# Performance work log

Hardware: AMD Instinct MI355X
Metric: run time of the kernel (lower is better)

## Reference

```python
import jax, jax.numpy as jnp
import numpy as np
import math

IN_CH = 256
RED_CH = 32  # max(256//8, 32)

def setup_inputs() -> dict:
    key = jax.random.key(0)
    k1, k2, k3, k4, k5 = jax.random.split(key, 5)
    x = jax.random.normal(k1, (2, IN_CH, 8, 28, 28), dtype=jnp.float32)
    # 1x1x1 Conv3d weights, kaiming-normal style scale (fan_out)
    def kaiming(k, shape):
        fan_out = shape[0]
        std = math.sqrt(2.0 / fan_out)
        return jax.random.normal(k, shape, dtype=jnp.float32) * std
    q_w = kaiming(k2, (RED_CH, IN_CH))
    k_w = kaiming(k3, (RED_CH, IN_CH))
    v_w = kaiming(k4, (RED_CH, IN_CH))
    out_w = kaiming(k5, (IN_CH, RED_CH))
    return {"x": x, "q_w": q_w, "k_w": k_w, "v_w": v_w, "out_w": out_w}

def reference(x, q_w, k_w, v_w, out_w):
    b, c, t, h, w = x.shape
    n = t * h * w
    xf = x.reshape(b, c, n)  # [B, C, N] (1x1x1 conv == channel matmul)
    q = jnp.einsum('rc,bcn->brn', q_w, xf)  # [B, Cr, N]
    k = jnp.einsum('rc,bcn->brn', k_w, xf)
    v = jnp.einsum('rc,bcn->brn', v_w, xf)
    scale = 1.0 / math.sqrt(RED_CH)
    attn = jnp.einsum('bri,brj->bij', q, k) * scale  # [B, N, N]
    attn = jax.nn.softmax(attn, axis=2)
    out = jnp.einsum('brj,bij->bri', v, attn)  # [B, Cr, N]
    out = jnp.einsum('cr,brn->bcn', out_w, out).reshape(b, c, t, h, w)
    return x + out
```

## Files before the change

kernel.cpp:

```cpp
#include <hip/hip_runtime.h>
#include <hip/hip_bf16.h>

#define NPOS 6272
#define NT   98
#define CIN  256
#define CR   32
#define BATCH 2
#define QS2  0.25503371989518595f
#define PPITCH 72

typedef short bf16x8s __attribute__((ext_vector_type(8)));
typedef short short4v __attribute__((ext_vector_type(4)));
typedef float f32x4   __attribute__((ext_vector_type(4)));
typedef unsigned short ushort_t;

__device__ __forceinline__ ushort_t f2bf(float f) {
    unsigned u = __builtin_bit_cast(unsigned, f);
    u += 0x7fff + ((u >> 16) & 1);
    return (ushort_t)(u >> 16);
}
__device__ __forceinline__ float bf2f(ushort_t h) {
    return __builtin_bit_cast(float, (unsigned)h << 16);
}
__device__ __forceinline__ ushort_t f2bf_hw(float f) {
    __bf16 b = (__bf16)f;
    return __builtin_bit_cast(ushort_t, b);
}

__global__ __launch_bounds__(256) void qkv_kernel(
    const float* __restrict__ x, const float* __restrict__ qw,
    const float* __restrict__ kw, const float* __restrict__ vw,
    ushort_t* __restrict__ Qh, ushort_t* __restrict__ Ql,
    ushort_t* __restrict__ Kh, ushort_t* __restrict__ Kl,
    ushort_t* __restrict__ Vt)
{
    const int b   = blockIdx.y;
    const int z   = blockIdx.z;
    const int nl  = threadIdx.x & 63;
    const int n   = blockIdx.x * 64 + nl;
    const int g   = __builtin_amdgcn_readfirstlane(threadIdx.x >> 6);
    const float* w  = (z == 0) ? qw : (z == 1) ? kw : vw;
    const float* xb = x + (size_t)b * CIN * NPOS + n;

    float acc[8];
#pragma unroll
    for (int i = 0; i < 8; ++i) acc[i] = 0.f;
#pragma unroll 8
    for (int c = 0; c < CIN; ++c) {
        float xv = xb[(size_t)c * NPOS];
#pragma unroll
        for (int i = 0; i < 8; ++i)
            acc[i] += w[(g * 8 + i) * CIN + c] * xv;
    }
    if (z == 2) {
#pragma unroll
        for (int i = 0; i < 8; ++i)
            Vt[((size_t)b * CR + g * 8 + i) * NPOS + n] = f2bf(acc[i]);
    } else {
        ushort_t* dh = (z == 0) ? Qh : Kh;
        ushort_t* dl = (z == 0) ? Ql : Kl;
        float s = (z == 0) ? QS2 : 1.0f;
        bf16x8s fh, fl;
#pragma unroll
        for (int i = 0; i < 8; ++i) {
            float v = acc[i] * s;
            ushort_t h = f2bf(v);
            fh[i] = (short)h;
            fl[i] = (short)f2bf(v - bf2f(h));
        }
        size_t off = ((size_t)b * NPOS + n) * CR + g * 8;
        *(bf16x8s*)(dh + off) = fh;
        *(bf16x8s*)(dl + off) = fl;
    }
}

__device__ __forceinline__ void load_tile(
    const ushort_t* __restrict__ Khb, const ushort_t* __restrict__ Klb,
    const ushort_t* __restrict__ Vtb, int j0, int col, int quad,
    bf16x8s* kh, bf16x8s* kl, bf16x8s* vb)
{
#pragma unroll
    for (int f = 0; f < 4; ++f) {
        kh[f] = *(const bf16x8s*)(Khb + (size_t)(j0 + f * 16 + col) * CR + quad * 8);
        kl[f] = *(const bf16x8s*)(Klb + (size_t)(j0 + f * 16 + col) * CR + quad * 8);
    }
#pragma unroll
    for (int k2 = 0; k2 < 2; ++k2)
#pragma unroll
        for (int c = 0; c < 2; ++c)
            vb[k2 * 2 + c] = *(const bf16x8s*)(
                Vtb + (size_t)(c * 16 + col) * NPOS + j0 + k2 * 32 + quad * 8);
}

__device__ __forceinline__ void compute_tile(
    const bf16x8s* kh, const bf16x8s* kl, const bf16x8s* vb,
    const bf16x8s* qbh, const bf16x8s* qbl,
    f32x4 (&oc)[2][2], float (&m_)[2], float (&l_)[2],
    ushort_t* pb, int col, int quad)
{
    f32x4 z4 = {0.f, 0.f, 0.f, 0.f};
#pragma unroll
    for (int h = 0; h < 2; ++h) {
        f32x4 sc[4];
#pragma unroll
        for (int f = 0; f < 4; ++f) {
            sc[f] = __builtin_amdgcn_mfma_f32_16x16x32_bf16(kl[f], qbh[h], z4, 0, 0, 0);
            sc[f] = __builtin_amdgcn_mfma_f32_16x16x32_bf16(kh[f], qbl[h], sc[f], 0, 0, 0);
            sc[f] = __builtin_amdgcn_mfma_f32_16x16x32_bf16(kh[f], qbh[h], sc[f], 0, 0, 0);
        }
        float a0 = fmaxf(fmaxf(sc[0][0], sc[0][1]), sc[0][2]);
        float a1 = fmaxf(fmaxf(sc[0][3], sc[1][0]), sc[1][1]);
        float a2 = fmaxf(fmaxf(sc[1][2], sc[1][3]), sc[2][0]);
        float a3 = fmaxf(fmaxf(sc[2][1], sc[2][2]), sc[2][3]);
        float a4 = fmaxf(fmaxf(sc[3][0], sc[3][1]), sc[3][2]);
        float b0 = fmaxf(fmaxf(a0, a1), a2);
        float b1 = fmaxf(fmaxf(a3, a4), sc[3][3]);
        float v  = fmaxf(b0, b1);
        v = fmaxf(v, __shfl_xor(v, 16));
        v = fmaxf(v, __shfl_xor(v, 32));
        float mo = m_[h];
        float mn = mo;
        if (!__all(v <= mo)) {
            mn = fmaxf(mo, v);
            float al = __builtin_amdgcn_exp2f(mo - mn);
            m_[h] = mn;
            l_[h] *= al;
#pragma unroll
            for (int r = 0; r < 4; ++r) { oc[h][0][r] *= al; oc[h][1][r] *= al; }
        }
        float lsum = 0.f;
#pragma unroll
        for (int f = 0; f < 4; ++f) {
            float p0 = __builtin_amdgcn_exp2f(sc[f][0] - mn);
            float p1 = __builtin_amdgcn_exp2f(sc[f][1] - mn);
            float p2 = __builtin_amdgcn_exp2f(sc[f][2] - mn);
            float p3 = __builtin_amdgcn_exp2f(sc[f][3] - mn);
            lsum += (p0 + p1) + (p2 + p3);
            short4v pk;
            pk[0] = (short)f2bf_hw(p0);
            pk[1] = (short)f2bf_hw(p1);
            pk[2] = (short)f2bf_hw(p2);
            pk[3] = (short)f2bf_hw(p3);
            *(short4v*)(&pb[h * 16 * PPITCH + col * PPITCH + f * 16 + quad * 4]) = pk;
        }
        l_[h] += lsum;
    }
#pragma unroll
    for (int h = 0; h < 2; ++h) {
#pragma unroll
        for (int k2 = 0; k2 < 2; ++k2) {
            bf16x8s pbo = *(const bf16x8s*)(
                &pb[h * 16 * PPITCH + col * PPITCH + k2 * 32 + quad * 8]);
            oc[h][0] = __builtin_amdgcn_mfma_f32_16x16x32_bf16(vb[k2 * 2 + 0], pbo, oc[h][0], 0, 0, 0);
            oc[h][1] = __builtin_amdgcn_mfma_f32_16x16x32_bf16(vb[k2 * 2 + 1], pbo, oc[h][1], 0, 0, 0);
        }
    }
}

template <int ITERS>
__global__ __launch_bounds__(128, 2) void attn_kernel(
    const ushort_t* __restrict__ Qh, const ushort_t* __restrict__ Ql,
    const ushort_t* __restrict__ Kh, const ushort_t* __restrict__ Kl,
    const ushort_t* __restrict__ Vt, ushort_t* __restrict__ Opart,
    float* __restrict__ Mp, float* __restrict__ Lp)
{
    __shared__ __align__(16) ushort_t pbuf[2 * 2 * 16 * PPITCH];

    const int lane = threadIdx.x & 63;
    const int wv   = threadIdx.x >> 6;
    const int col  = lane & 15;
    const int quad = lane >> 4;
    const int b    = blockIdx.z;
    const int s    = blockIdx.y;
    const int qw0  = blockIdx.x * 64 + wv * 32;
    ushort_t* pb   = &pbuf[wv * 2 * 16 * PPITCH];

    const ushort_t* Qhb = Qh + (size_t)b * NPOS * CR;
    const ushort_t* Qlb = Ql + (size_t)b * NPOS * CR;
    const ushort_t* Khb = Kh + (size_t)b * NPOS * CR;
    const ushort_t* Klb = Kl + (size_t)b * NPOS * CR;
    const ushort_t* Vtb = Vt + (size_t)b * CR * NPOS;

    bf16x8s qbh[2], qbl[2];
    qbh[0] = *(const bf16x8s*)(Qhb + (size_t)(qw0 + col) * CR + quad * 8);
    qbh[1] = *(const bf16x8s*)(Qhb + (size_t)(qw0 + 16 + col) * CR + quad * 8);
    qbl[0] = *(const bf16x8s*)(Qlb + (size_t)(qw0 + col) * CR + quad * 8);
    qbl[1] = *(const bf16x8s*)(Qlb + (size_t)(qw0 + 16 + col) * CR + quad * 8);

    f32x4 oc[2][2];
#pragma unroll
    for (int h = 0; h < 2; ++h)
#pragma unroll
        for (int c = 0; c < 2; ++c)
#pragma unroll
            for (int r = 0; r < 4; ++r) oc[h][c][r] = 0.f;
    float m_[2] = { -1e30f, -1e30f };
    float l_[2] = { 0.f, 0.f };

    if constexpr (ITERS <= 14) {
        bf16x8s kh2[2][4], kl2[2][4], vb2[2][4];
        load_tile(Khb, Klb, Vtb, s * ITERS * 64, col, quad,
                  kh2[0], kl2[0], vb2[0]);
#pragma unroll
        for (int it = 0; it < ITERS; ++it) {
            const int cur = it & 1;
            if (it + 1 < ITERS)
                load_tile(Khb, Klb, Vtb, (s * ITERS + it + 1) * 64, col, quad,
                          kh2[cur ^ 1], kl2[cur ^ 1], vb2[cur ^ 1]);
            compute_tile(kh2[cur], kl2[cur], vb2[cur], qbh, qbl, oc, m_, l_,
                         pb, col, quad);
        }
    } else {
        for (int it = 0; it < ITERS; ++it) {
            bf16x8s kh[4], kl[4], vb[4];
            load_tile(Khb, Klb, Vtb, (s * ITERS + it) * 64, col, quad, kh, kl, vb);
            compute_tile(kh, kl, vb, qbh, qbl, oc, m_, l_, pb, col, quad);
        }
    }

#pragma unroll
    for (int h = 0; h < 2; ++h) {
        float l = l_[h];
        l += __shfl_xor(l, 16);
        l += __shfl_xor(l, 32);
        l_[h] = l;
    }

    const size_t sb = (size_t)(s * BATCH + b);
    ushort_t* Ob = Opart + sb * CR * NPOS;
#pragma unroll
    for (int h = 0; h < 2; ++h)
#pragma unroll
        for (int c = 0; c < 2; ++c)
#pragma unroll
            for (int r = 0; r < 4; ++r) {
                int ch = c * 16 + quad * 4 + r;
                Ob[(size_t)ch * NPOS + qw0 + h * 16 + col] = f2bf(oc[h][c][r]);
            }
    if (quad == 0) {
#pragma unroll
        for (int h = 0; h < 2; ++h) {
            Mp[sb * NPOS + qw0 + h * 16 + col] = m_[h];
            Lp[sb * NPOS + qw0 + h * 16 + col] = l_[h];
        }
    }
}

template <int S_>
__global__ __launch_bounds__(256) void merge_kernel(
    const ushort_t* __restrict__ Opart, const float* __restrict__ Mp,
    const float* __restrict__ Lp, float* __restrict__ Omrg)
{
    const int b  = blockIdx.y;
    const int z  = blockIdx.z;
    const int nl = threadIdx.x & 63;
    const int n  = blockIdx.x * 64 + nl;
    const int g  = __builtin_amdgcn_readfirstlane(threadIdx.x >> 6);
    const int r  = z * 4 + g;

    float mv[S_];
    float mg = -1e30f;
#pragma unroll
    for (int s = 0; s < S_; ++s) {
        mv[s] = Mp[(size_t)(s * BATCH + b) * NPOS + n];
        mg = fmaxf(mg, mv[s]);
    }
    float lg = 0.f, acc = 0.f;
#pragma unroll
    for (int s = 0; s < S_; ++s) {
        size_t sb = (size_t)(s * BATCH + b);
        float w = __builtin_amdgcn_exp2f(mv[s] - mg);
        lg  += w * Lp[sb * NPOS + n];
        acc += w * bf2f(Opart[(sb * CR + r) * NPOS + n]);
    }
    Omrg[((size_t)b * CR + r) * NPOS + n] = acc / lg;
}

__global__ __launch_bounds__(256) void proj_kernel(
    const float* __restrict__ Omrg, const float* __restrict__ ow,
    const float* __restrict__ x, float* __restrict__ y)
{
    const int b  = blockIdx.y;
    const int z  = blockIdx.z;
    const int nl = threadIdx.x & 63;
    const int n  = blockIdx.x * 64 + nl;
    const int g  = __builtin_amdgcn_readfirstlane(threadIdx.x >> 6);

    float o[CR];
#pragma unroll
    for (int r = 0; r < CR; ++r)
        o[r] = Omrg[((size_t)b * CR + r) * NPOS + n];

    const float* xb = x + (size_t)b * CIN * NPOS + n;
    float*       yb = y + (size_t)b * CIN * NPOS + n;
    const int c0 = z * 32 + g * 8;
#pragma unroll
    for (int cc = 0; cc < 8; ++cc) {
        int c = c0 + cc;
        float acc = xb[(size_t)c * NPOS];
#pragma unroll
        for (int r = 0; r < CR; ++r) acc += ow[c * CR + r] * o[r];
        yb[(size_t)c * NPOS] = acc;
    }
}

extern "C" void kernel_launch(void* const* d_in, const int* in_sizes, int n_in,
                              void* d_out, int out_size, void* d_ws, size_t ws_size,
                              hipStream_t stream)
{
    const float* x  = (const float*)d_in[0];
    const float* qw = (const float*)d_in[1];
    const float* kw = (const float*)d_in[2];
    const float* vw = (const float*)d_in[3];
    const float* ow = (const float*)d_in[4];
    float* out = (float*)d_out;

    const size_t qkvN = (size_t)BATCH * CR * NPOS;
    const int s_cand[4] = {7, 14, 2, 1};
    int S = 1;
    for (int i = 0; i < 4; ++i) {
        int Sc = s_cand[i];
        size_t need = 5 * qkvN * sizeof(ushort_t)
                    + qkvN * sizeof(float)
                    + (size_t)Sc * qkvN * sizeof(ushort_t)
                    + 2 * (size_t)Sc * BATCH * NPOS * sizeof(float);
        if (need <= ws_size) { S = Sc; break; }
    }
    ushort_t* Qh = (ushort_t*)d_ws;
    ushort_t* Ql = Qh + qkvN;
    ushort_t* Kh = Ql + qkvN;
    ushort_t* Kl = Kh + qkvN;
    ushort_t* Vt = Kl + qkvN;
    float* Omrg  = (float*)(Vt + qkvN);
    ushort_t* Op = (ushort_t*)(Omrg + qkvN);
    float* Mp    = (float*)(Op + (size_t)S * qkvN);
    float* Lp    = Mp + (size_t)S * BATCH * NPOS;

    qkv_kernel<<<dim3(NT, BATCH, 3), 256, 0, stream>>>(x, qw, kw, vw,
                                                       Qh, Ql, Kh, Kl, Vt);
    dim3 ag(NT, S, BATCH);
    switch (S) {
        case 14: attn_kernel<7> <<<ag, 128, 0, stream>>>(Qh, Ql, Kh, Kl, Vt, Op, Mp, Lp); break;
        case 7:  attn_kernel<14><<<ag, 128, 0, stream>>>(Qh, Ql, Kh, Kl, Vt, Op, Mp, Lp); break;
        case 2:  attn_kernel<49><<<ag, 128, 0, stream>>>(Qh, Ql, Kh, Kl, Vt, Op, Mp, Lp); break;
        default: attn_kernel<98><<<ag, 128, 0, stream>>>(Qh, Ql, Kh, Kl, Vt, Op, Mp, Lp); break;
    }
    dim3 mg(NT, BATCH, 8);
    switch (S) {
        case 14: merge_kernel<14><<<mg, 256, 0, stream>>>(Op, Mp, Lp, Omrg); break;
        case 7:  merge_kernel<7> <<<mg, 256, 0, stream>>>(Op, Mp, Lp, Omrg); break;
        case 2:  merge_kernel<2> <<<mg, 256, 0, stream>>>(Op, Mp, Lp, Omrg); break;
        default: merge_kernel<1> <<<mg, 256, 0, stream>>>(Op, Mp, Lp, Omrg); break;
    }
    proj_kernel<<<dim3(NT, BATCH, 8), 256, 0, stream>>>(Omrg, ow, x, out);
}
```

Before: 144.4 us.

## Fuse split-softmax merge with output projection and restructure KV double-buffer loop

Merges the partial-softmax combine kernel and the output projection into one kernel that stages merged outputs in LDS, removing the Omrg round-trip through global memory and one launch. Each block now covers 128 output channels instead of 32, so the merge work is redone twice per position rather than eight times. The attention loop is rewritten as a non-unrolled ping-pong with two named register buffers, meant to keep prefetch overlap while cutting code size and register pressure. The merge step is still recomputed once per z-block, and the projection grid is smaller.

```diff
diff --git a/kernel.cpp b/kernel.cpp
--- a/kernel.cpp
+++ b/kernel.cpp
@@ -197,20 +197,22 @@
     float m_[2] = { -1e30f, -1e30f };
     float l_[2] = { 0.f, 0.f };
 
-    if constexpr (ITERS <= 14) {
-        bf16x8s kh2[2][4], kl2[2][4], vb2[2][4];
-        load_tile(Khb, Klb, Vtb, s * ITERS * 64, col, quad,
-                  kh2[0], kl2[0], vb2[0]);
-#pragma unroll
-        for (int it = 0; it < ITERS; ++it) {
-            const int cur = it & 1;
-            if (it + 1 < ITERS)
-                load_tile(Khb, Klb, Vtb, (s * ITERS + it + 1) * 64, col, quad,
-                          kh2[cur ^ 1], kl2[cur ^ 1], vb2[cur ^ 1]);
-            compute_tile(kh2[cur], kl2[cur], vb2[cur], qbh, qbl, oc, m_, l_,
-                         pb, col, quad);
-        }
+    if constexpr (ITERS >= 4 && (ITERS % 2) == 0) {
+        bf16x8s kA[4], lA[4], vA[4], kB[4], lB[4], vB[4];
+        const int base = s * ITERS;
+        load_tile(Khb, Klb, Vtb, base * 64, col, quad, kA, lA, vA);
+#pragma unroll 1
+        for (int it = 0; it < ITERS - 2; it += 2) {
+            load_tile(Khb, Klb, Vtb, (base + it + 1) * 64, col, quad, kB, lB, vB);
+            compute_tile(kA, lA, vA, qbh, qbl, oc, m_, l_, pb, col, quad);
+            load_tile(Khb, Klb, Vtb, (base + it + 2) * 64, col, quad, kA, lA, vA);
+            compute_tile(kB, lB, vB, qbh, qbl, oc, m_, l_, pb, col, quad);
+        }
+        load_tile(Khb, Klb, Vtb, (base + ITERS - 1) * 64, col, quad, kB, lB, vB);
+        compute_tile(kA, lA, vA, qbh, qbl, oc, m_, l_, pb, col, quad);
+        compute_tile(kB, lB, vB, qbh, qbl, oc, m_, l_, pb, col, quad);
     } else {
+#pragma unroll 1
         for (int it = 0; it < ITERS; ++it) {
             bf16x8s kh[4], kl[4], vb[4];
             load_tile(Khb, Klb, Vtb, (s * ITERS + it) * 64, col, quad, kh, kl, vb);
@@ -247,55 +249,52 @@
 }
 
 template <int S_>
-__global__ __launch_bounds__(256) void merge_kernel(
+__global__ __launch_bounds__(256) void mergeproj_kernel(
     const ushort_t* __restrict__ Opart, const float* __restrict__ Mp,
-    const float* __restrict__ Lp, float* __restrict__ Omrg)
-{
+    const float* __restrict__ Lp, const float* __restrict__ ow,
+    const float* __restrict__ x, float* __restrict__ y)
+{
+    __shared__ float o_lds[CR][64];
     const int b  = blockIdx.y;
     const int z  = blockIdx.z;
     const int nl = threadIdx.x & 63;
     const int n  = blockIdx.x * 64 + nl;
     const int g  = __builtin_amdgcn_readfirstlane(threadIdx.x >> 6);
-    const int r  = z * 4 + g;
-
-    float mv[S_];
+
+    float mv[S_], wv_[S_];
     float mg = -1e30f;
 #pragma unroll
     for (int s = 0; s < S_; ++s) {
         mv[s] = Mp[(size_t)(s * BATCH + b) * NPOS + n];
         mg = fmaxf(mg, mv[s]);
     }
-    float lg = 0.f, acc = 0.f;
+    float lg = 0.f;
 #pragma unroll
     for (int s = 0; s < S_; ++s) {
-        size_t sb = (size_t)(s * BATCH + b);
-        float w = __builtin_amdgcn_exp2f(mv[s] - mg);
-        lg  += w * Lp[sb * NPOS + n];
-        acc += w * bf2f(Opart[(sb * CR + r) * NPOS + n]);
-    }
-    Omrg[((size_t)b * CR + r) * NPOS + n] = acc / lg;
-}
-
-__global__ __launch_bounds__(256) void proj_kernel(
-    const float* __restrict__ Omrg, const float* __restrict__ ow,
-    const float* __restrict__ x, float* __restrict__ y)
-{
-    const int b  = blockIdx.y;
-    const int z  = blockIdx.z;
-    const int nl = threadIdx.x & 63;
-    const int n  = blockIdx.x * 64 + nl;
-    const int g  = __builtin_amdgcn_readfirstlane(threadIdx.x >> 6);
+        wv_[s] = __builtin_amdgcn_exp2f(mv[s] - mg);
+        lg += wv_[s] * Lp[(size_t)(s * BATCH + b) * NPOS + n];
+    }
+    float inv = 1.0f / lg;
+#pragma unroll
+    for (int rr = 0; rr < 8; ++rr) {
+        int r = g * 8 + rr;
+        float acc = 0.f;
+#pragma unroll
+        for (int s = 0; s < S_; ++s)
+            acc += wv_[s] * bf2f(Opart[((size_t)(s * BATCH + b) * CR + r) * NPOS + n]);
+        o_lds[r][nl] = acc * inv;
+    }
+    __syncthreads();
 
     float o[CR];
 #pragma unroll
-    for (int r = 0; r < CR; ++r)
-        o[r] = Omrg[((size_t)b * CR + r) * NPOS + n];
+    for (int r = 0; r < CR; ++r) o[r] = o_lds[r][nl];
 
     const float* xb = x + (size_t)b * CIN * NPOS + n;
     float*       yb = y + (size_t)b * CIN * NPOS + n;
-    const int c0 = z * 32 + g * 8;
-#pragma unroll
-    for (int cc = 0; cc < 8; ++cc) {
+    const int c0 = z * 128 + g * 32;
+#pragma unroll 8
+    for (int cc = 0; cc < 32; ++cc) {
         int c = c0 + cc;
         float acc = xb[(size_t)c * NPOS];
 #pragma unroll
@@ -345,12 +344,11 @@
         case 2:  attn_kernel<49><<<ag, 128, 0, stream>>>(Qh, Ql, Kh, Kl, Vt, Op, Mp, Lp); break;
         default: attn_kernel<98><<<ag, 128, 0, stream>>>(Qh, Ql, Kh, Kl, Vt, Op, Mp, Lp); break;
     }
-    dim3 mg(NT, BATCH, 8);
+    dim3 mpg(NT, BATCH, 2);
     switch (S) {
-        case 14: merge_kernel<14><<<mg, 256, 0, stream>>>(Op, Mp, Lp, Omrg); break;
-        case 7:  merge_kernel<7> <<<mg, 256, 0, stream>>>(Op, Mp, Lp, Omrg); break;
-        case 2:  merge_kernel<2> <<<mg, 256, 0, stream>>>(Op, Mp, Lp, Omrg); break;
-        default: merge_kernel<1> <<<mg, 256, 0, stream>>>(Op, Mp, Lp, Omrg); break;
-    }
-    proj_kernel<<<dim3(NT, BATCH, 8), 256, 0, stream>>>(Omrg, ow, x, out);
-}
+        case 14: mergeproj_kernel<14><<<mpg, 256, 0, stream>>>(Op, Mp, Lp, ow, x, out); break;
+        case 7:  mergeproj_kernel<7> <<<mpg, 256, 0, stream>>>(Op, Mp, Lp, ow, x, out); break;
+        case 2:  mergeproj_kernel<2> <<<mpg, 256, 0, stream>>>(Op, Mp, Lp, ow, x, out); break;
+        default: mergeproj_kernel<1> <<<mpg, 256, 0, stream>>>(Op, Mp, Lp, ow, x, out); break;
+    }
+}
```

Result: slower. 150.2 us (+4.0%).

## Fuse QKV, attention, merge and projection into one cooperative persistent kernel

Applied to the files above, without the earlier changes.

Replaces the four kernel launches with a single cooperative launch of a persistent grid of 512 blocks. The blocks walk wave-level work units for each stage and separate the stages with grid-wide syncs. The aim is to remove launch gaps and tail effects between the dependent kernels. The attention loop is also rewritten as a non-unrolled two-buffer ping-pong, replacing the fully unrolled double buffering. Risks are grid-sync overhead, lower occupancy (256 threads with launch bounds of 2 blocks) for the attention stage, and work imbalance because the unit counts are not multiples of the wave count.

```diff
diff --git a/kernel.cpp b/kernel.cpp
--- a/kernel.cpp
+++ b/kernel.cpp
@@ -1,5 +1,8 @@
 #include <hip/hip_runtime.h>
 #include <hip/hip_bf16.h>
+#include <hip/hip_cooperative_groups.h>
+
+namespace cg = cooperative_groups;
 
 #define NPOS 6272
 #define NT   98
@@ -8,6 +11,7 @@
 #define BATCH 2
 #define QS2  0.25503371989518595f
 #define PPITCH 72
+#define SATT 7
 
 typedef short bf16x8s __attribute__((ext_vector_type(8)));
 typedef short short4v __attribute__((ext_vector_type(4)));
@@ -27,18 +31,16 @@
     return __builtin_bit_cast(ushort_t, b);
 }
 
-__global__ __launch_bounds__(256) void qkv_kernel(
+
+__device__ __forceinline__ void qkv_unit(
     const float* __restrict__ x, const float* __restrict__ qw,
     const float* __restrict__ kw, const float* __restrict__ vw,
     ushort_t* __restrict__ Qh, ushort_t* __restrict__ Ql,
     ushort_t* __restrict__ Kh, ushort_t* __restrict__ Kl,
-    ushort_t* __restrict__ Vt)
-{
-    const int b   = blockIdx.y;
-    const int z   = blockIdx.z;
-    const int nl  = threadIdx.x & 63;
-    const int n   = blockIdx.x * 64 + nl;
-    const int g   = __builtin_amdgcn_readfirstlane(threadIdx.x >> 6);
+    ushort_t* __restrict__ Vt,
+    int nt, int b, int z, int g, int nl)
+{
+    const int n = nt * 64 + nl;
     const float* w  = (z == 0) ? qw : (z == 1) ? kw : vw;
     const float* xb = x + (size_t)b * CIN * NPOS + n;
 
@@ -158,6 +160,222 @@
 }
 
 template <int ITERS>
+__device__ __forceinline__ void attn_unit(
+    const ushort_t* __restrict__ Qh, const ushort_t* __restrict__ Ql,
+    const ushort_t* __restrict__ Kh, const ushort_t* __restrict__ Kl,
+    const ushort_t* __restrict__ Vt, ushort_t* __restrict__ Opart,
+    float* __restrict__ Mp, float* __restrict__ Lp,
+    int nt, int s, int b, int wq, ushort_t* pb, int lane)
+{
+    const int col  = lane & 15;
+    const int quad = lane >> 4;
+    const int qw0  = nt * 64 + wq * 32;
+
+    const ushort_t* Qhb = Qh + (size_t)b * NPOS * CR;
+    const ushort_t* Qlb = Ql + (size_t)b * NPOS * CR;
+    const ushort_t* Khb = Kh + (size_t)b * NPOS * CR;
+    const ushort_t* Klb = Kl + (size_t)b * NPOS * CR;
+    const ushort_t* Vtb = Vt + (size_t)b * CR * NPOS;
+
+    bf16x8s qbh[2], qbl[2];
+    qbh[0] = *(const bf16x8s*)(Qhb + (size_t)(qw0 + col) * CR + quad * 8);
+    qbh[1] = *(const bf16x8s*)(Qhb + (size_t)(qw0 + 16 + col) * CR + quad * 8);
+    qbl[0] = *(const bf16x8s*)(Qlb + (size_t)(qw0 + col) * CR + quad * 8);
+    qbl[1] = *(const bf16x8s*)(Qlb + (size_t)(qw0 + 16 + col) * CR + quad * 8);
+
+    f32x4 oc[2][2];
+#pragma unroll
+    for (int h = 0; h < 2; ++h)
+#pragma unroll
+        for (int c = 0; c < 2; ++c)
+#pragma unroll
+            for (int r = 0; r < 4; ++r) oc[h][c][r] = 0.f;
+    float m_[2] = { -1e30f, -1e30f };
+    float l_[2] = { 0.f, 0.f };
+
+    const int base = s * ITERS;
+    if constexpr (ITERS >= 4 && (ITERS % 2) == 0) {
+        bf16x8s kA[4], lA[4], vA[4], kB[4], lB[4], vB[4];
+        load_tile(Khb, Klb, Vtb, base * 64, col, quad, kA, lA, vA);
+#pragma unroll 1
+        for (int it = 0; it < ITERS - 2; it += 2) {
+            load_tile(Khb, Klb, Vtb, (base + it + 1) * 64, col, quad, kB, lB, vB);
+            compute_tile(kA, lA, vA, qbh, qbl, oc, m_, l_, pb, col, quad);
+            load_tile(Khb, Klb, Vtb, (base + it + 2) * 64, col, quad, kA, lA, vA);
+            compute_tile(kB, lB, vB, qbh, qbl, oc, m_, l_, pb, col, quad);
+        }
+        load_tile(Khb, Klb, Vtb, (base + ITERS - 1) * 64, col, quad, kB, lB, vB);
+        compute_tile(kA, lA, vA, qbh, qbl, oc, m_, l_, pb, col, quad);
+        compute_tile(kB, lB, vB, qbh, qbl, oc, m_, l_, pb, col, quad);
+    } else {
+#pragma unroll 1
+        for (int it = 0; it < ITERS; ++it) {
+            bf16x8s kh[4], kl[4], vb[4];
+            load_tile(Khb, Klb, Vtb, (base + it) * 64, col, quad, kh, kl, vb);
+            compute_tile(kh, kl, vb, qbh, qbl, oc, m_, l_, pb, col, quad);
+        }
+    }
+
+#pragma unroll
+    for (int h = 0; h < 2; ++h) {
+        float l = l_[h];
+        l += __shfl_xor(l, 16);
+        l += __shfl_xor(l, 32);
+        l_[h] = l;
+    }
+
+    const size_t sb = (size_t)(s * BATCH + b);
+    ushort_t* Ob = Opart + sb * CR * NPOS;
+#pragma unroll
+    for (int h = 0; h < 2; ++h)
+#pragma unroll
+        for (int c = 0; c < 2; ++c)
+#pragma unroll
+            for (int r = 0; r < 4; ++r) {
+                int ch = c * 16 + quad * 4 + r;
+                Ob[(size_t)ch * NPOS + qw0 + h * 16 + col] = f2bf(oc[h][c][r]);
+            }
+    if (quad == 0) {
+#pragma unroll
+        for (int h = 0; h < 2; ++h) {
+            Mp[sb * NPOS + qw0 + h * 16 + col] = m_[h];
+            Lp[sb * NPOS + qw0 + h * 16 + col] = l_[h];
+        }
+    }
+}
+
+template <int S_>
+__device__ __forceinline__ void merge_unit(
+    const ushort_t* __restrict__ Opart, const float* __restrict__ Mp,
+    const float* __restrict__ Lp, float* __restrict__ Omrg,
+    int nt, int b, int z, int g, int nl)
+{
+    const int n = nt * 64 + nl;
+    const int r = z * 4 + g;
+    float mv[S_];
+    float mg = -1e30f;
+#pragma unroll
+    for (int s = 0; s < S_; ++s) {
+        mv[s] = Mp[(size_t)(s * BATCH + b) * NPOS + n];
+        mg = fmaxf(mg, mv[s]);
+    }
+    float lg = 0.f, acc = 0.f;
+#pragma unroll
+    for (int s = 0; s < S_; ++s) {
+        size_t sb = (size_t)(s * BATCH + b);
+        float w = __builtin_amdgcn_exp2f(mv[s] - mg);
+        lg  += w * Lp[sb * NPOS + n];
+        acc += w * bf2f(Opart[(sb * CR + r) * NPOS + n]);
+    }
+    Omrg[((size_t)b * CR + r) * NPOS + n] = acc / lg;
+}
+
+__device__ __forceinline__ void proj_unit(
+    const float* __restrict__ Omrg, const float* __restrict__ ow,
+    const float* __restrict__ x, float* __restrict__ y,
+    int nt, int b, int z, int g, int nl)
+{
+    const int n = nt * 64 + nl;
+    float o[CR];
+#pragma unroll
+    for (int r = 0; r < CR; ++r)
+        o[r] = Omrg[((size_t)b * CR + r) * NPOS + n];
+
+    const float* xb = x + (size_t)b * CIN * NPOS + n;
+    float*       yb = y + (size_t)b * CIN * NPOS + n;
+    const int c0 = z * 32 + g * 8;
+#pragma unroll
+    for (int cc = 0; cc < 8; ++cc) {
+        int c = c0 + cc;
+        float acc = xb[(size_t)c * NPOS];
+#pragma unroll
+        for (int r = 0; r < CR; ++r) acc += ow[c * CR + r] * o[r];
+        yb[(size_t)c * NPOS] = acc;
+    }
+}
+
+#define FUSED_BLOCKS 512
+#define FUSED_WAVES  (FUSED_BLOCKS * 4)
+
+__global__ __launch_bounds__(256, 2) void fused_kernel(
+    const float* __restrict__ x, const float* __restrict__ qw,
+    const float* __restrict__ kw, const float* __restrict__ vw,
+    const float* __restrict__ ow,
+    ushort_t* __restrict__ Qh, ushort_t* __restrict__ Ql,
+    ushort_t* __restrict__ Kh, ushort_t* __restrict__ Kl,
+    ushort_t* __restrict__ Vt, ushort_t* __restrict__ Opart,
+    float* __restrict__ Mp, float* __restrict__ Lp,
+    float* __restrict__ Omrg, float* __restrict__ y)
+{
+    cg::grid_group grid = cg::this_grid();
+    __shared__ __align__(16) ushort_t pbuf[4 * 2 * 16 * PPITCH];
+
+    const int nl   = threadIdx.x & 63;
+    const int wv4  = __builtin_amdgcn_readfirstlane(threadIdx.x >> 6);
+    const int gw0  = blockIdx.x * 4 + wv4;
+
+#pragma unroll 1
+    for (int u = gw0; u < 2352; u += FUSED_WAVES) {
+        int t  = u;
+        const int nt = t % 98; t /= 98;
+        const int g  = t & 3;  t >>= 2;
+        const int b  = t & 1;  t >>= 1;
+        const int z  = t;
+        qkv_unit(x, qw, kw, vw, Qh, Ql, Kh, Kl, Vt, nt, b, z, g, nl);
+    }
+    grid.sync();
+
+    {
+        ushort_t* pb = &pbuf[wv4 * 2 * 16 * PPITCH];
+#pragma unroll 1
+        for (int u = gw0; u < 98 * SATT * BATCH * 2; u += FUSED_WAVES) {
+            int t  = u;
+            const int nt = t % 98; t /= 98;
+            const int wq = t & 1;  t >>= 1;
+            const int b  = t & 1;  t >>= 1;
+            const int s  = t;
+            attn_unit<98 / SATT>(Qh, Ql, Kh, Kl, Vt, Opart, Mp, Lp,
+                                 nt, s, b, wq, pb, nl);
+        }
+    }
+    grid.sync();
+
+#pragma unroll 1
+    for (int u = gw0; u < 6272; u += FUSED_WAVES) {
+        int t  = u;
+        const int nt = t % 98; t /= 98;
+        const int g  = t & 3;  t >>= 2;
+        const int b  = t & 1;  t >>= 1;
+        const int z  = t;
+        merge_unit<SATT>(Opart, Mp, Lp, Omrg, nt, b, z, g, nl);
+    }
+    grid.sync();
+
+#pragma unroll 1
+    for (int u = gw0; u < 6272; u += FUSED_WAVES) {
+        int t  = u;
+        const int nt = t % 98; t /= 98;
+        const int g  = t & 3;  t >>= 2;
+        const int b  = t & 1;  t >>= 1;
+        const int z  = t;
+        proj_unit(Omrg, ow, x, y, nt, b, z, g, nl);
+    }
+}
+
+__global__ __launch_bounds__(256) void qkv_kernel(
+    const float* __restrict__ x, const float* __restrict__ qw,
+    const float* __restrict__ kw, const float* __restrict__ vw,
+    ushort_t* __restrict__ Qh, ushort_t* __restrict__ Ql,
+    ushort_t* __restrict__ Kh, ushort_t* __restrict__ Kl,
+    ushort_t* __restrict__ Vt)
+{
+    qkv_unit(x, qw, kw, vw, Qh, Ql, Kh, Kl, Vt,
+             blockIdx.x, blockIdx.y, blockIdx.z,
+             __builtin_amdgcn_readfirstlane(threadIdx.x >> 6),
+             threadIdx.x & 63);
+}
+
+template <int ITERS>
 __global__ __launch_bounds__(128, 2) void attn_kernel(
     const ushort_t* __restrict__ Qh, const ushort_t* __restrict__ Ql,
     const ushort_t* __restrict__ Kh, const ushort_t* __restrict__ Kl,
@@ -165,85 +383,10 @@
     float* __restrict__ Mp, float* __restrict__ Lp)
 {
     __shared__ __align__(16) ushort_t pbuf[2 * 2 * 16 * PPITCH];
-
-    const int lane = threadIdx.x & 63;
-    const int wv   = threadIdx.x >> 6;
-    const int col  = lane & 15;
-    const int quad = lane >> 4;
-    const int b    = blockIdx.z;
-    const int s    = blockIdx.y;
-    const int qw0  = blockIdx.x * 64 + wv * 32;
-    ushort_t* pb   = &pbuf[wv * 2 * 16 * PPITCH];
-
-    const ushort_t* Qhb = Qh + (size_t)b * NPOS * CR;
-    const ushort_t* Qlb = Ql + (size_t)b * NPOS * CR;
-    const ushort_t* Khb = Kh + (size_t)b * NPOS * CR;
-    const ushort_t* Klb = Kl + (size_t)b * NPOS * CR;
-    const ushort_t* Vtb = Vt + (size_t)b * CR * NPOS;
-
-    bf16x8s qbh[2], qbl[2];
-    qbh[0] = *(const bf16x8s*)(Qhb + (size_t)(qw0 + col) * CR + quad * 8);
-    qbh[1] = *(const bf16x8s*)(Qhb + (size_t)(qw0 + 16 + col) * CR + quad * 8);
-    qbl[0] = *(const bf16x8s*)(Qlb + (size_t)(qw0 + col) * CR + quad * 8);
-    qbl[1] = *(const bf16x8s*)(Qlb + (size_t)(qw0 + 16 + col) * CR + quad * 8);
-
-    f32x4 oc[2][2];
-#pragma unroll
-    for (int h = 0; h < 2; ++h)
-#pragma unroll
-        for (int c = 0; c < 2; ++c)
-#pragma unroll
-            for (int r = 0; r < 4; ++r) oc[h][c][r] = 0.f;
-    float m_[2] = { -1e30f, -1e30f };
-    float l_[2] = { 0.f, 0.f };
-
-    if constexpr (ITERS <= 14) {
-        bf16x8s kh2[2][4], kl2[2][4], vb2[2][4];
-        load_tile(Khb, Klb, Vtb, s * ITERS * 64, col, quad,
-                  kh2[0], kl2[0], vb2[0]);
-#pragma unroll
-        for (int it = 0; it < ITERS; ++it) {
-            const int cur = it & 1;
-            if (it + 1 < ITERS)
-                load_tile(Khb, Klb, Vtb, (s * ITERS + it + 1) * 64, col, quad,
-                          kh2[cur ^ 1], kl2[cur ^ 1], vb2[cur ^ 1]);
-            compute_tile(kh2[cur], kl2[cur], vb2[cur], qbh, qbl, oc, m_, l_,
-                         pb, col, quad);
-        }
-    } else {
-        for (int it = 0; it < ITERS; ++it) {
-            bf16x8s kh[4], kl[4], vb[4];
-            load_tile(Khb, Klb, Vtb, (s * ITERS + it) * 64, col, quad, kh, kl, vb);
-            compute_tile(kh, kl, vb, qbh, qbl, oc, m_, l_, pb, col, quad);
-        }
-    }
-
-#pragma unroll
-    for (int h = 0; h < 2; ++h) {
-        float l = l_[h];
-        l += __shfl_xor(l, 16);
-        l += __shfl_xor(l, 32);
-        l_[h] = l;
-    }
-
-    const size_t sb = (size_t)(s * BATCH + b);
-    ushort_t* Ob = Opart + sb * CR * NPOS;
-#pragma unroll
-    for (int h = 0; h < 2; ++h)
-#pragma unroll
-        for (int c = 0; c < 2; ++c)
-#pragma unroll
-            for (int r = 0; r < 4; ++r) {
-                int ch = c * 16 + quad * 4 + r;
-                Ob[(size_t)ch * NPOS + qw0 + h * 16 + col] = f2bf(oc[h][c][r]);
-            }
-    if (quad == 0) {
-#pragma unroll
-        for (int h = 0; h < 2; ++h) {
-            Mp[sb * NPOS + qw0 + h * 16 + col] = m_[h];
-            Lp[sb * NPOS + qw0 + h * 16 + col] = l_[h];
-        }
-    }
+    const int wv = __builtin_amdgcn_readfirstlane(threadIdx.x >> 6);
+    attn_unit<ITERS>(Qh, Ql, Kh, Kl, Vt, Opart, Mp, Lp,
+                     blockIdx.x, blockIdx.y, blockIdx.z, wv,
+                     &pbuf[wv * 2 * 16 * PPITCH], threadIdx.x & 63);
 }
 
 template <int S_>
@@ -251,57 +394,20 @@
     const ushort_t* __restrict__ Opart, const float* __restrict__ Mp,
     const float* __restrict__ Lp, float* __restrict__ Omrg)
 {
-    const int b  = blockIdx.y;
-    const int z  = blockIdx.z;
-    const int nl = threadIdx.x & 63;
-    const int n  = blockIdx.x * 64 + nl;
-    const int g  = __builtin_amdgcn_readfirstlane(threadIdx.x >> 6);
-    const int r  = z * 4 + g;
-
-    float mv[S_];
-    float mg = -1e30f;
-#pragma unroll
-    for (int s = 0; s < S_; ++s) {
-        mv[s] = Mp[(size_t)(s * BATCH + b) * NPOS + n];
-        mg = fmaxf(mg, mv[s]);
-    }
-    float lg = 0.f, acc = 0.f;
-#pragma unroll
-    for (int s = 0; s < S_; ++s) {
-        size_t sb = (size_t)(s * BATCH + b);
-        float w = __builtin_amdgcn_exp2f(mv[s] - mg);
-        lg  += w * Lp[sb * NPOS + n];
-        acc += w * bf2f(Opart[(sb * CR + r) * NPOS + n]);
-    }
-    Omrg[((size_t)b * CR + r) * NPOS + n] = acc / lg;
+    merge_unit<S_>(Opart, Mp, Lp, Omrg,
+                   blockIdx.x, blockIdx.y, blockIdx.z,
+                   __builtin_amdgcn_readfirstlane(threadIdx.x >> 6),
+                   threadIdx.x & 63);
 }
 
 __global__ __launch_bounds__(256) void proj_kernel(
     const float* __restrict__ Omrg, const float* __restrict__ ow,
     const float* __restrict__ x, float* __restrict__ y)
 {
-    const int b  = blockIdx.y;
-    const int z  = blockIdx.z;
-    const int nl = threadIdx.x & 63;
-    const int n  = blockIdx.x * 64 + nl;
-    const int g  = __builtin_amdgcn_readfirstlane(threadIdx.x >> 6);
-
-    float o[CR];
-#pragma unroll
-    for (int r = 0; r < CR; ++r)
-        o[r] = Omrg[((size_t)b * CR + r) * NPOS + n];
-
-    const float* xb = x + (size_t)b * CIN * NPOS + n;
-    float*       yb = y + (size_t)b * CIN * NPOS + n;
-    const int c0 = z * 32 + g * 8;
-#pragma unroll
-    for (int cc = 0; cc < 8; ++cc) {
-        int c = c0 + cc;
-        float acc = xb[(size_t)c * NPOS];
-#pragma unroll
-        for (int r = 0; r < CR; ++r) acc += ow[c * CR + r] * o[r];
-        yb[(size_t)c * NPOS] = acc;
-    }
+    proj_unit(Omrg, ow, x, y,
+              blockIdx.x, blockIdx.y, blockIdx.z,
+              __builtin_amdgcn_readfirstlane(threadIdx.x >> 6),
+              threadIdx.x & 63);
 }
 
 extern "C" void kernel_launch(void* const* d_in, const int* in_sizes, int n_in,
@@ -316,41 +422,59 @@
     float* out = (float*)d_out;
 
     const size_t qkvN = (size_t)BATCH * CR * NPOS;
-    const int s_cand[4] = {7, 14, 2, 1};
-    int S = 1;
-    for (int i = 0; i < 4; ++i) {
-        int Sc = s_cand[i];
-        size_t need = 5 * qkvN * sizeof(ushort_t)
-                    + qkvN * sizeof(float)
-                    + (size_t)Sc * qkvN * sizeof(ushort_t)
-                    + 2 * (size_t)Sc * BATCH * NPOS * sizeof(float);
-        if (need <= ws_size) { S = Sc; break; }
-    }
+
+    size_t needS7 = 5 * qkvN * sizeof(ushort_t)
+                  + qkvN * sizeof(float)
+                  + (size_t)SATT * qkvN * sizeof(ushort_t)
+                  + 2 * (size_t)SATT * BATCH * NPOS * sizeof(float);
+
     ushort_t* Qh = (ushort_t*)d_ws;
     ushort_t* Ql = Qh + qkvN;
     ushort_t* Kh = Ql + qkvN;
     ushort_t* Kl = Kh + qkvN;
     ushort_t* Vt = Kl + qkvN;
-    float* Omrg  = (float*)(Vt + qkvN);
-    ushort_t* Op = (ushort_t*)(Omrg + qkvN);
-    float* Mp    = (float*)(Op + (size_t)S * qkvN);
-    float* Lp    = Mp + (size_t)S * BATCH * NPOS;
-
-    qkv_kernel<<<dim3(NT, BATCH, 3), 256, 0, stream>>>(x, qw, kw, vw,
-                                                       Qh, Ql, Kh, Kl, Vt);
-    dim3 ag(NT, S, BATCH);
-    switch (S) {
-        case 14: attn_kernel<7> <<<ag, 128, 0, stream>>>(Qh, Ql, Kh, Kl, Vt, Op, Mp, Lp); break;
-        case 7:  attn_kernel<14><<<ag, 128, 0, stream>>>(Qh, Ql, Kh, Kl, Vt, Op, Mp, Lp); break;
-        case 2:  attn_kernel<49><<<ag, 128, 0, stream>>>(Qh, Ql, Kh, Kl, Vt, Op, Mp, Lp); break;
-        default: attn_kernel<98><<<ag, 128, 0, stream>>>(Qh, Ql, Kh, Kl, Vt, Op, Mp, Lp); break;
-    }
-    dim3 mg(NT, BATCH, 8);
-    switch (S) {
-        case 14: merge_kernel<14><<<mg, 256, 0, stream>>>(Op, Mp, Lp, Omrg); break;
-        case 7:  merge_kernel<7> <<<mg, 256, 0, stream>>>(Op, Mp, Lp, Omrg); break;
-        case 2:  merge_kernel<2> <<<mg, 256, 0, stream>>>(Op, Mp, Lp, Omrg); break;
-        default: merge_kernel<1> <<<mg, 256, 0, stream>>>(Op, Mp, Lp, Omrg); break;
-    }
-    proj_kernel<<<dim3(NT, BATCH, 8), 256, 0, stream>>>(Omrg, ow, x, out);
-}
+
+    if (needS7 <= ws_size) {
+        float* Omrg  = (float*)(Vt + qkvN);
+        ushort_t* Op = (ushort_t*)(Omrg + qkvN);
+        float* Mp    = (float*)(Op + (size_t)SATT * qkvN);
+        float* Lp    = Mp + (size_t)SATT * BATCH * NPOS;
+
+        int dev = 0;
+        hipGetDevice(&dev);
+        int coop = 0;
+        hipDeviceGetAttribute(&coop, hipDeviceAttributeCooperativeLaunch, dev);
+        if (coop) {
+            void* args[] = {
+                (void*)&x,  (void*)&qw, (void*)&kw, (void*)&vw, (void*)&ow,
+                (void*)&Qh, (void*)&Ql, (void*)&Kh, (void*)&Kl, (void*)&Vt,
+                (void*)&Op, (void*)&Mp, (void*)&Lp, (void*)&Omrg, (void*)&out
+            };
+            hipError_t rc = hipLaunchCooperativeKernel(
+                (const void*)fused_kernel, dim3(FUSED_BLOCKS), dim3(256),
+                args, 0, stream);
+            if (rc == hipSuccess) return;
+            (void)hipGetLastError();
+        }
+        qkv_kernel<<<dim3(NT, BATCH, 3), 256, 0, stream>>>(x, qw, kw, vw,
+                                                           Qh, Ql, Kh, Kl, Vt);
+        attn_kernel<98 / SATT><<<dim3(NT, SATT, BATCH), 128, 0, stream>>>(
+            Qh, Ql, Kh, Kl, Vt, Op, Mp, Lp);
+        merge_kernel<SATT><<<dim3(NT, BATCH, 8), 256, 0, stream>>>(Op, Mp, Lp, Omrg);
+        proj_kernel<<<dim3(NT, BATCH, 8), 256, 0, stream>>>(Omrg, ow, x, out);
+        return;
+    }
+
+    {
+        float* Omrg  = (float*)(Vt + qkvN);
+        ushort_t* Op = (ushort_t*)(Omrg + qkvN);
+        float* Mp    = (float*)(Op + qkvN);
+        float* Lp    = Mp + (size_t)BATCH * NPOS;
+        qkv_kernel<<<dim3(NT, BATCH, 3), 256, 0, stream>>>(x, qw, kw, vw,
+                                                           Qh, Ql, Kh, Kl, Vt);
+        attn_kernel<98><<<dim3(NT, 1, BATCH), 128, 0, stream>>>(
+            Qh, Ql, Kh, Kl, Vt, Op, Mp, Lp);
+        merge_kernel<1><<<dim3(NT, BATCH, 8), 256, 0, stream>>>(Op, Mp, Lp, Omrg);
+        proj_kernel<<<dim3(NT, BATCH, 8), 256, 0, stream>>>(Omrg, ow, x, out);
+    }
+}
```

After: 360.8 us. 150% more time.
